# Performance work log

Hardware: AMD Instinct MI355X
Metric: run time of the kernel (lower is better)

The kernel has to match this reference:

```python
import jax, jax.numpy as jnp
import numpy as np

HIDDEN = 50


def _lstm_layer(x_tbi, w_ih, w_hh, b_ih, b_hh):
    """One LSTM layer, PyTorch gate order (i, f, g, o).
    x_tbi: [T, B, in]; returns h sequence [T, B, H]."""
    B = x_tbi.shape[1]
    H = w_hh.shape[1]
    # Precompute input projections for all timesteps at once (one big GEMM).
    x_proj = jnp.einsum('tbi,gi->tbg', x_tbi, w_ih) + b_ih + b_hh  # [T, B, 4H]

    def step(carry, xp):
        h, c = carry
        gates = xp + h @ w_hh.T  # [B, 4H]
        i, f, g, o = jnp.split(gates, 4, axis=-1)
        i = jax.nn.sigmoid(i)
        f = jax.nn.sigmoid(f)
        g = jnp.tanh(g)
        o = jax.nn.sigmoid(o)
        c = f * c + i * g
        h = o * jnp.tanh(c)
        return (h, c), h

    h0 = jnp.zeros((B, H), dtype=x_tbi.dtype)
    c0 = jnp.zeros((B, H), dtype=x_tbi.dtype)
    _, hs = jax.lax.scan(step, (h0, c0), x_proj)
    return hs  # [T, B, H]


def setup_inputs() -> dict:
    key = jax.random.key(0)
    ks = jax.random.split(key, 12)
    B, T, I, H = 2048, 512, 12, HIDDEN
    s_in = 1.0 / np.sqrt(H)  # PyTorch LSTM init scale
    inp = {
        'x': jax.random.normal(ks[0], (B, T, I), dtype=jnp.float32),
        'w_ih0': jax.random.uniform(ks[1], (4 * H, I), jnp.float32, -s_in, s_in),
        'w_hh0': jax.random.uniform(ks[2], (4 * H, H), jnp.float32, -s_in, s_in),
        'b_ih0': jax.random.uniform(ks[3], (4 * H,), jnp.float32, -s_in, s_in),
        'b_hh0': jax.random.uniform(ks[4], (4 * H,), jnp.float32, -s_in, s_in),
        'w_ih1': jax.random.uniform(ks[5], (4 * H, H), jnp.float32, -s_in, s_in),
        'w_hh1': jax.random.uniform(ks[6], (4 * H, H), jnp.float32, -s_in, s_in),
        'b_ih1': jax.random.uniform(ks[7], (4 * H,), jnp.float32, -s_in, s_in),
        'b_hh1': jax.random.uniform(ks[8], (4 * H,), jnp.float32, -s_in, s_in),
        'w_out': jax.random.uniform(ks[9], (1, H), jnp.float32, -s_in, s_in),
        'b_out': jax.random.uniform(ks[10], (1,), jnp.float32, -s_in, s_in),
    }
    return inp


def reference(x, w_ih0, w_hh0, b_ih0, b_hh0, w_ih1, w_hh1, b_ih1, b_hh1, w_out, b_out):
    # x: [B, T, I] (batch_first). Scan works over leading time axis.
    x_tbi = jnp.transpose(x, (1, 0, 2))  # [T, B, I]
    h1 = _lstm_layer(x_tbi, w_ih0, w_hh0, b_ih0, b_hh0)  # [T, B, H]
    h2 = _lstm_layer(h1, w_ih1, w_hh1, b_ih1, b_hh1)     # [T, B, H]
    last = h2[-1]                                         # r_out[:, -1, :] -> [B, H]
    logits = last @ w_out.T + b_out                       # [B, 1]
    return jax.nn.sigmoid(logits)
```

## Files before the change

kernel.cpp:

```cpp
#include <hip/hip_runtime.h>

#define TT   512
#define BI   12
#define HH   50
#define BB   8
#define BTOT 2048
#define LOG2E 1.4426950408889634f


typedef _Float16 half8 __attribute__((ext_vector_type(8)));
typedef float    f4    __attribute__((ext_vector_type(4)));

__device__ __forceinline__ float sigm_(float v) {
    return __builtin_amdgcn_rcpf(1.f + __builtin_amdgcn_exp2f(v * (-LOG2E)));
}
__device__ __forceinline__ float dppmerge_(float a0, float a1) {
    int r = __builtin_amdgcn_update_dpp(__builtin_bit_cast(int, a0),
                                        __builtin_bit_cast(int, a1),
                                        0x128, 0xF, 0xC, false);
    return __builtin_bit_cast(float, r);
}

__launch_bounds__(1024)
__global__ void lstm2_kernel(const float* __restrict__ x,
                             const float* __restrict__ w_ih0, const float* __restrict__ w_hh0,
                             const float* __restrict__ b_ih0, const float* __restrict__ b_hh0,
                             const float* __restrict__ w_ih1, const float* __restrict__ w_hh1,
                             const float* __restrict__ b_ih1, const float* __restrict__ b_hh1,
                             const float* __restrict__ w_out, const float* __restrict__ b_out,
                             float* __restrict__ out)
{
    const int tid   = threadIdx.x;
    const int wv    = tid >> 6;
    const int lane  = tid & 63;
    const int layer = wv >> 3;
    const int w8    = wv & 7;
    const int b0    = blockIdx.x * BB;
    const int t0     = (w8 < 5) ? 2 * w8 : (5 + w8);
    const int ntiles = (w8 < 5) ? 2 : 1;

    __shared__ __align__(16) _Float16 B0s[2][64 * 16];
    __shared__ __align__(16) _Float16 B1s[2][64 * 16];

    const int m = lane & 15;
    const int q = lane >> 4;
    half8 af[2][4];
    #pragma unroll
    for (int s = 0; s < 2; s++) {
        #pragma unroll
        for (int kb = 0; kb < 4; kb++) {
            #pragma unroll
            for (int j = 0; j < 8; j++) {
                float v = 0.f;
                if (s < ntiles && (layer == 1 || kb < 2)) {
                    const int T  = t0 + s;
                    const int u  = T * 4 + (m >> 2);
                    const int g  = m & 3;
                    const int kg = kb * 32 + q * 8 + j;
                    if (u < HH) {
                        const int r = g * HH + u;
                        if (layer == 0) {
                            if      (kg < 50)  v = w_hh0[r * HH + kg];
                            else if (kg < 62)  v = w_ih0[r * BI + (kg - 50)];
                            else if (kg == 62) v = b_ih0[r] + b_hh0[r];
                        } else {
                            if      (kg < 50)               v = w_ih1[r * HH + kg];
                            else if (kg >= 64 && kg < 114)  v = w_hh1[r * HH + (kg - 64)];
                            else if (kg == 126)             v = b_ih1[r] + b_hh1[r];
                        }
                        v *= (g == 2) ? (2.f * LOG2E) : (-LOG2E);
                    }
                }
                af[s][kb][j] = (_Float16)v;
            }
        }
    }

    for (int i = tid; i < 2 * 64 * 16; i += 1024) {
        (&B0s[0][0])[i] = (_Float16)0.f;
        (&B1s[0][0])[i] = (_Float16)0.f;
    }
    __syncthreads();
    if (tid < 16) {
        B0s[0][7 * 128 + tid * 8 + 6] = (_Float16)1.f;
        B0s[1][7 * 128 + tid * 8 + 6] = (_Float16)1.f;
        B1s[0][7 * 128 + tid * 8 + 6] = (_Float16)1.f;
        B1s[1][7 * 128 + tid * 8 + 6] = (_Float16)1.f;
    }
    const int xb = tid / 12, xi = tid - xb * 12;
    const int xrow = 50 + xi;
    const int xoff = (xrow >> 3) * 128 + xb * 8 + (xrow & 7);
    const size_t xbase = ((size_t)(b0 + xb) * TT) * BI + xi;
    if (tid < 96)
        B0s[0][xoff] = (_Float16)x[xbase];
    __syncthreads();

    const int n16  = lane & 15;
    const int slot = n16 >> 3;
    const int bcol = n16 & 7;
    const int u_m  = (t0 + slot) * 4 + q;
    const bool wvalid = (u_m < HH) && (slot == 0 || ntiles == 2);
    float cm = 0.f;

    const _Float16* rd0[2] = { &B0s[0][0] + lane * 8, &B0s[1][0] + lane * 8 };
    const _Float16* rd1[2] = { &B1s[0][0] + lane * 8, &B1s[1][0] + lane * 8 };
    const int offA = (u_m >> 3) * 128 + bcol * 8 + (u_m & 7);
    _Float16* wAp[2] = { (layer ? &B1s[0][0] : &B0s[0][0]) + offA,
                         (layer ? &B1s[1][0] : &B0s[1][0]) + offA };
    _Float16* xdp[2] = { &B0s[0][0] + xoff, &B0s[1][0] + xoff };

    const f4 fzero = {0.f, 0.f, 0.f, 0.f};

    const float* xq = x + xbase + BI;
    float xhold = 0.f;
    if (tid < 96) xhold = *xq;
    xq += BI;

#define BARRIER()                                                             \
    asm volatile("s_waitcnt lgkmcnt(0)" ::: "memory");                        \
    __builtin_amdgcn_s_barrier();                                             \
    asm volatile("" ::: "memory");

#define STEP(P, DOL0, DOL1, DOST, DOLD)                                       \
  {                                                                           \
    float xnew = 0.f;                                                         \
    if ((DOLD) && tid < 96) xnew = *xq;                                       \
    if ((DOST) && tid < 96) *xdp[1 - (P)] = (_Float16)xhold;                  \
    if ((layer == 0) ? (DOL0) : (DOL1)) {                                     \
      const half8 bf0 = *(const half8*)(rd0[P]);                              \
      const half8 bf1 = *(const half8*)(rd0[P] + 512);                        \
      f4 acc0, acc1 = fzero;                                                  \
      if (layer == 0) {                                                       \
        acc0 = __builtin_amdgcn_mfma_f32_16x16x32_f16(af[0][0], bf0, fzero, 0, 0, 0); \
        acc0 = __builtin_amdgcn_mfma_f32_16x16x32_f16(af[0][1], bf1, acc0, 0, 0, 0);  \
        if (ntiles > 1) {                                                     \
          acc1 = __builtin_amdgcn_mfma_f32_16x16x32_f16(af[1][0], bf0, fzero, 0, 0, 0); \
          acc1 = __builtin_amdgcn_mfma_f32_16x16x32_f16(af[1][1], bf1, acc1, 0, 0, 0);  \
        }                                                                     \
      } else {                                                                \
        const half8 bf2 = *(const half8*)(rd1[P]);                            \
        const half8 bf3 = *(const half8*)(rd1[P] + 512);                      \
        f4 a0  = __builtin_amdgcn_mfma_f32_16x16x32_f16(af[0][0], bf0, fzero, 0, 0, 0); \
        f4 a0b = __builtin_amdgcn_mfma_f32_16x16x32_f16(af[0][1], bf1, fzero, 0, 0, 0); \
        a0  = __builtin_amdgcn_mfma_f32_16x16x32_f16(af[0][2], bf2, a0,  0, 0, 0);      \
        a0b = __builtin_amdgcn_mfma_f32_16x16x32_f16(af[0][3], bf3, a0b, 0, 0, 0);      \
        acc0 = a0 + a0b;                                                      \
        if (ntiles > 1) {                                                     \
          f4 a1  = __builtin_amdgcn_mfma_f32_16x16x32_f16(af[1][0], bf0, fzero, 0, 0, 0); \
          f4 a1b = __builtin_amdgcn_mfma_f32_16x16x32_f16(af[1][1], bf1, fzero, 0, 0, 0); \
          a1  = __builtin_amdgcn_mfma_f32_16x16x32_f16(af[1][2], bf2, a1,  0, 0, 0);      \
          a1b = __builtin_amdgcn_mfma_f32_16x16x32_f16(af[1][3], bf3, a1b, 0, 0, 0);      \
          acc1 = a1 + a1b;                                                    \
        }                                                                     \
      }                                                                       \
      f4 am;                                                                  \
      _Pragma("unroll")                                                       \
      for (int i = 0; i < 4; i++) am[i] = dppmerge_(acc0[i], acc1[i]);        \
      const float eI = __builtin_amdgcn_exp2f(am[0]);                         \
      const float eF = __builtin_amdgcn_exp2f(am[1]);                         \
      const float eG = __builtin_amdgcn_exp2f(am[2]);                         \
      const float eO = __builtin_amdgcn_exp2f(am[3]);                         \
      const float dI = 1.f + eI, dF = 1.f + eF;                               \
      const float dG = 1.f + eG, dO = 1.f + eO;                               \
      const float pIG = dI * dG;                                              \
      const float num = __builtin_fmaf(cm, pIG, (eG - 1.f) * dF);             \
      cm = num * __builtin_amdgcn_rcpf(dF * pIG);                             \
      const float uu = fminf(cm * (2.f * LOG2E), 60.f);                       \
      const float eC = __builtin_amdgcn_exp2f(uu);                            \
      const float h  = (eC - 1.f) * __builtin_amdgcn_rcpf(dO * (1.f + eC));   \
      if (wvalid) *wAp[1 - (P)] = (_Float16)h;                                \
    }                                                                         \
    if (DOLD) { xhold = xnew; xq += BI; }                                     \
    BARRIER()                                                                 \
  }

    STEP(0, 1, 0, 1, 1)
    STEP(1, 1, 1, 1, 1)
    #pragma unroll 1
    for (int it = 0; it < 254; ++it) {
        STEP(0, 1, 1, 1, 1)
        STEP(1, 1, 1, 1, 1)
    }
    STEP(0, 1, 1, 1, 0)
    STEP(1, 1, 1, 0, 0)
    STEP(0, 0, 1, 0, 0)
#undef STEP
#undef BARRIER

    if (tid < BB) {
        float s = b_out[0];
        #pragma unroll
        for (int u = 0; u < HH; u++) {
            s += w_out[u] * (float)B1s[1][(u >> 3) * 128 + tid * 8 + (u & 7)];
        }
        out[b0 + tid] = sigm_(s);
    }
}

extern "C" void kernel_launch(void* const* d_in, const int* in_sizes, int n_in,
                              void* d_out, int out_size, void* d_ws, size_t ws_size,
                              hipStream_t stream) {
    const float* x     = (const float*)d_in[0];
    const float* w_ih0 = (const float*)d_in[1];
    const float* w_hh0 = (const float*)d_in[2];
    const float* b_ih0 = (const float*)d_in[3];
    const float* b_hh0 = (const float*)d_in[4];
    const float* w_ih1 = (const float*)d_in[5];
    const float* w_hh1 = (const float*)d_in[6];
    const float* b_ih1 = (const float*)d_in[7];
    const float* b_hh1 = (const float*)d_in[8];
    const float* w_out = (const float*)d_in[9];
    const float* b_out = (const float*)d_in[10];
    float* out = (float*)d_out;

    dim3 grid(BTOT / BB);
    dim3 block(1024);
    lstm2_kernel<<<grid, block, 0, stream>>>(x, w_ih0, w_hh0, b_ih0, b_hh0,
                                             w_ih1, w_hh1, b_ih1, b_hh1,
                                             w_out, b_out, out);
}
```

Measured before the change: 373.6 us.

## Split each LSTM step into two barrier phases interleaving layer MFMA and activations

Each timestep becomes two phases. In one phase layer-0 warps run their MFMAs while layer-1 warps compute activations from the previous phase's results. In the other, layer-0 warps do activations while layer-1 warps run MFMAs. The goal is to balance matrix and transcendental work across the waves in the block so the MFMA and VALU units are busy together instead of each step waiting on the slowest chain. It doubles the number of block barriers per timestep and adds a trailing phase plus a final __syncthreads.

```diff
diff --git a/kernel.cpp b/kernel.cpp
--- a/kernel.cpp
+++ b/kernel.cpp
@@ -111,40 +111,78 @@
 
     const f4 fzero = {0.f, 0.f, 0.f, 0.f};
 
+    f4 acc0v = fzero, acc1v = fzero;
+    f4 am1   = fzero;
+    float xnewP = 0.f;
+
     const float* xq = x + xbase + BI;
     float xhold = 0.f;
     if (tid < 96) xhold = *xq;
     xq += BI;
 
-#define BARRIER()                                                             \
+#define BARX()                                                                \
     asm volatile("s_waitcnt lgkmcnt(0)" ::: "memory");                        \
     __builtin_amdgcn_s_barrier();                                             \
     asm volatile("" ::: "memory");
 
-#define STEP(P, DOL0, DOL1, DOST, DOLD)                                       \
+#define DOACT(AM, WPTR)                                                       \
   {                                                                           \
-    float xnew = 0.f;                                                         \
-    if ((DOLD) && tid < 96) xnew = *xq;                                       \
+    const float eI = __builtin_amdgcn_exp2f((AM)[0]);                         \
+    const float eF = __builtin_amdgcn_exp2f((AM)[1]);                         \
+    const float eG = __builtin_amdgcn_exp2f((AM)[2]);                         \
+    const float eO = __builtin_amdgcn_exp2f((AM)[3]);                         \
+    const float dI = 1.f + eI, dF = 1.f + eF;                                 \
+    const float dG = 1.f + eG, dO = 1.f + eO;                                 \
+    const float pIG = dI * dG;                                                \
+    const float num = __builtin_fmaf(cm, pIG, (eG - 1.f) * dF);               \
+    cm = num * __builtin_amdgcn_rcpf(dF * pIG);                               \
+    const float uu = fminf(cm * (2.f * LOG2E), 60.f);                         \
+    const float eC = __builtin_amdgcn_exp2f(uu);                              \
+    const float h_ = (eC - 1.f) * __builtin_amdgcn_rcpf(dO * (1.f + eC));     \
+    if (wvalid) *(WPTR) = (_Float16)h_;                                       \
+  }
+
+#define PHASEA(P, A0, A1, DOLD)                                               \
+  {                                                                           \
+    if ((DOLD) && tid < 96) xnewP = *xq;                                      \
+    if (layer == 0) {                                                         \
+      if (A0) {                                                               \
+        const half8 bf0 = *(const half8*)(rd0[P]);                            \
+        const half8 bf1 = *(const half8*)(rd0[P] + 512);                      \
+        acc0v = __builtin_amdgcn_mfma_f32_16x16x32_f16(af[0][0], bf0, fzero, 0, 0, 0); \
+        acc0v = __builtin_amdgcn_mfma_f32_16x16x32_f16(af[0][1], bf1, acc0v, 0, 0, 0); \
+        if (ntiles > 1) {                                                     \
+          acc1v = __builtin_amdgcn_mfma_f32_16x16x32_f16(af[1][0], bf0, fzero, 0, 0, 0); \
+          acc1v = __builtin_amdgcn_mfma_f32_16x16x32_f16(af[1][1], bf1, acc1v, 0, 0, 0); \
+        }                                                                     \
+      }                                                                       \
+    } else {                                                                  \
+      if (A1) DOACT(am1, wAp[P])                                              \
+    }                                                                         \
+    BARX()                                                                    \
+  }
+
+#define PHASEB(P, B0, B1, DOST, DOLD)                                         \
+  {                                                                           \
     if ((DOST) && tid < 96) *xdp[1 - (P)] = (_Float16)xhold;                  \
-    if ((layer == 0) ? (DOL0) : (DOL1)) {                                     \
-      const half8 bf0 = *(const half8*)(rd0[P]);                              \
-      const half8 bf1 = *(const half8*)(rd0[P] + 512);                        \
-      f4 acc0, acc1 = fzero;                                                  \
-      if (layer == 0) {                                                       \
-        acc0 = __builtin_amdgcn_mfma_f32_16x16x32_f16(af[0][0], bf0, fzero, 0, 0, 0); \
-        acc0 = __builtin_amdgcn_mfma_f32_16x16x32_f16(af[0][1], bf1, acc0, 0, 0, 0);  \
-        if (ntiles > 1) {                                                     \
-          acc1 = __builtin_amdgcn_mfma_f32_16x16x32_f16(af[1][0], bf0, fzero, 0, 0, 0); \
-          acc1 = __builtin_amdgcn_mfma_f32_16x16x32_f16(af[1][1], bf1, acc1, 0, 0, 0);  \
-        }                                                                     \
-      } else {                                                                \
+    if (layer == 0) {                                                         \
+      if (B0) {                                                               \
+        f4 am;                                                                \
+        _Pragma("unroll")                                                     \
+        for (int i = 0; i < 4; i++) am[i] = dppmerge_(acc0v[i], acc1v[i]);    \
+        DOACT(am, wAp[1 - (P)])                                               \
+      }                                                                       \
+    } else {                                                                  \
+      if (B1) {                                                               \
+        const half8 bf0 = *(const half8*)(rd0[P]);                            \
+        const half8 bf1 = *(const half8*)(rd0[P] + 512);                      \
         const half8 bf2 = *(const half8*)(rd1[P]);                            \
         const half8 bf3 = *(const half8*)(rd1[P] + 512);                      \
         f4 a0  = __builtin_amdgcn_mfma_f32_16x16x32_f16(af[0][0], bf0, fzero, 0, 0, 0); \
         f4 a0b = __builtin_amdgcn_mfma_f32_16x16x32_f16(af[0][1], bf1, fzero, 0, 0, 0); \
         a0  = __builtin_amdgcn_mfma_f32_16x16x32_f16(af[0][2], bf2, a0,  0, 0, 0);      \
         a0b = __builtin_amdgcn_mfma_f32_16x16x32_f16(af[0][3], bf3, a0b, 0, 0, 0);      \
-        acc0 = a0 + a0b;                                                      \
+        f4 acc0 = a0 + a0b, acc1 = fzero;                                     \
         if (ntiles > 1) {                                                     \
           f4 a1  = __builtin_amdgcn_mfma_f32_16x16x32_f16(af[1][0], bf0, fzero, 0, 0, 0); \
           f4 a1b = __builtin_amdgcn_mfma_f32_16x16x32_f16(af[1][1], bf1, fzero, 0, 0, 0); \
@@ -152,40 +190,31 @@
           a1b = __builtin_amdgcn_mfma_f32_16x16x32_f16(af[1][3], bf3, a1b, 0, 0, 0);      \
           acc1 = a1 + a1b;                                                    \
         }                                                                     \
+        _Pragma("unroll")                                                     \
+        for (int i = 0; i < 4; i++) am1[i] = dppmerge_(acc0[i], acc1[i]);     \
       }                                                                       \
-      f4 am;                                                                  \
-      _Pragma("unroll")                                                       \
-      for (int i = 0; i < 4; i++) am[i] = dppmerge_(acc0[i], acc1[i]);        \
-      const float eI = __builtin_amdgcn_exp2f(am[0]);                         \
-      const float eF = __builtin_amdgcn_exp2f(am[1]);                         \
-      const float eG = __builtin_amdgcn_exp2f(am[2]);                         \
-      const float eO = __builtin_amdgcn_exp2f(am[3]);                         \
-      const float dI = 1.f + eI, dF = 1.f + eF;                               \
-      const float dG = 1.f + eG, dO = 1.f + eO;                               \
-      const float pIG = dI * dG;                                              \
-      const float num = __builtin_fmaf(cm, pIG, (eG - 1.f) * dF);             \
-      cm = num * __builtin_amdgcn_rcpf(dF * pIG);                             \
-      const float uu = fminf(cm * (2.f * LOG2E), 60.f);                       \
-      const float eC = __builtin_amdgcn_exp2f(uu);                            \
-      const float h  = (eC - 1.f) * __builtin_amdgcn_rcpf(dO * (1.f + eC));   \
-      if (wvalid) *wAp[1 - (P)] = (_Float16)h;                                \
     }                                                                         \
-    if (DOLD) { xhold = xnew; xq += BI; }                                     \
-    BARRIER()                                                                 \
+    if (DOLD) { xhold = xnewP; xq += BI; }                                    \
+    BARX()                                                                    \
   }
 
-    STEP(0, 1, 0, 1, 1)
-    STEP(1, 1, 1, 1, 1)
+    PHASEA(0, 1, 0, 1) PHASEB(0, 1, 0, 1, 1)
+    PHASEA(1, 1, 0, 1) PHASEB(1, 1, 1, 1, 1)
     #pragma unroll 1
     for (int it = 0; it < 254; ++it) {
-        STEP(0, 1, 1, 1, 1)
-        STEP(1, 1, 1, 1, 1)
-    }
-    STEP(0, 1, 1, 1, 0)
-    STEP(1, 1, 1, 0, 0)
-    STEP(0, 0, 1, 0, 0)
-#undef STEP
-#undef BARRIER
+        PHASEA(0, 1, 1, 1) PHASEB(0, 1, 1, 1, 1)
+        PHASEA(1, 1, 1, 1) PHASEB(1, 1, 1, 1, 1)
+    }
+    PHASEA(0, 1, 1, 0) PHASEB(0, 1, 1, 1, 0)
+    PHASEA(1, 1, 1, 0) PHASEB(1, 1, 1, 0, 0)
+    PHASEA(0, 0, 1, 0) PHASEB(0, 0, 1, 0, 0)
+    PHASEA(1, 0, 1, 0)
+#undef PHASEA
+#undef PHASEB
+#undef DOACT
+#undef BARX
+
+    __syncthreads();
 
     if (tid < BB) {
         float s = b_out[0];
```

After: 403.9 us. 8.1% more time.
